# Optimization experiments

Measured on AMD Instinct MI355X. Metric: run time of the kernel, lower is better.

Reference implementation:

```python
import jax, jax.numpy as jnp
import numpy as np

B, S, D = 4, 2048, 2048
E = 64           # num_experts
TOPK = 2         # num_experts_per_token


def setup_inputs() -> dict:
    key = jax.random.key(0)
    k1, k2, k3 = jax.random.split(key, 3)
    x_real = jax.random.normal(k1, (B, S, D), dtype=jnp.float32)
    x_imag = jax.random.normal(k2, (B, S, D), dtype=jnp.float32)
    # flax Dense: kernel [in_features, out_features] with lecun_normal-ish scale
    W = jax.random.normal(k3, (2 * D, E), dtype=jnp.float32) / np.sqrt(2.0 * D)
    b = jnp.zeros((E,), dtype=jnp.float32)
    return {"x_real": x_real, "x_imag": x_imag, "W": W, "b": b}


def reference(x_real, x_imag, W, b):
    # amp = |x|, phase = angle(x) for x = x_real + i*x_imag
    amp = jnp.hypot(x_real, x_imag)                 # [B,S,D]
    phase = jnp.arctan2(x_imag, x_real)             # [B,S,D]
    routing_input = jnp.concatenate([amp, phase], axis=-1)  # [B,S,2D]
    scores = jnp.einsum('bsf,fe->bse', routing_input, W) + b  # [B,S,E]
    probs = jax.nn.softmax(scores, axis=-1)
    top_k_probs, top_k_indices = jax.lax.top_k(probs, TOPK)   # [B,S,K]
    top_k_probs = top_k_probs / jnp.sum(top_k_probs, axis=-1, keepdims=True)
    return (top_k_probs, top_k_indices)
```

## Files before the change

kernel.cpp:

```cpp
#include <hip/hip_runtime.h>
#include <math.h>

#define NTOK 8192
#define DD   2048
#define EE   64
#define STRIP 16
#define NKH 8
#define DSLICE (DD/NKH)
#define NCH (DSLICE/32)
#define PROB_N (NTOK*2)
#define F_SSTRIDE (128*4*64*8)

typedef __bf16 bf16x8 __attribute__((ext_vector_type(8)));
typedef float  f32x4  __attribute__((ext_vector_type(4)));
typedef unsigned short u16x8 __attribute__((ext_vector_type(8)));

__device__ __forceinline__ unsigned short bf16_rne(float x, float& rep) {
    unsigned u = __builtin_bit_cast(unsigned, x);
    unsigned r = u + 0x7FFFu + ((u >> 16) & 1u);
    unsigned short h = (unsigned short)(r >> 16);
    rep = __builtin_bit_cast(float, (unsigned)h << 16);
    return h;
}
__device__ __forceinline__ void split3(float x, unsigned short& h1,
                                       unsigned short& h2, unsigned short& h3) {
    float f1, f2, f3;
    h1 = bf16_rne(x, f1);
    float r1 = x - f1;
    h2 = bf16_rne(r1, f2);
    float r2 = r1 - f2;
    h3 = bf16_rne(r2, f3);
}

__global__ __launch_bounds__(256) void wsplit(const float* __restrict__ W,
                                              unsigned short* __restrict__ F) {
    const int g  = blockIdx.x * 256 + threadIdx.x;
    const int e  = g & 63;
    const int q  = g >> 6;
    const int d0 = q * 4;
    const int nt = e >> 4;
    const int k  = d0 & 31;
    const int lane = (k >> 3) * 16 + (e & 15);
    const int j0 = k & 7;
    const int ck = 2 * (d0 >> 5);

    unsigned short ah[3][4], ph[3][4];
    #pragma unroll
    for (int i = 0; i < 4; ++i) {
        split3(W[(size_t)(d0 + i) * EE + e],      ah[0][i], ah[1][i], ah[2][i]);
        split3(W[(size_t)(DD + d0 + i) * EE + e], ph[0][i], ph[1][i], ph[2][i]);
    }
    #pragma unroll
    for (int s = 0; s < 3; ++s) {
        ushort4 va = make_ushort4(ah[s][0], ah[s][1], ah[s][2], ah[s][3]);
        ushort4 vp = make_ushort4(ph[s][0], ph[s][1], ph[s][2], ph[s][3]);
        *(ushort4*)&F[(size_t)(((s * 128 + ck)     * 4 + nt) * 64 + lane) * 8 + j0] = va;
        *(ushort4*)&F[(size_t)(((s * 128 + ck + 1) * 4 + nt) * 64 + lane) * 8 + j0] = vp;
    }
}

__global__ __launch_bounds__(512, 4) void gemm_topk(
    const float* __restrict__ xr, const float* __restrict__ xi,
    const unsigned short* __restrict__ F, const float* __restrict__ bias,
    float* __restrict__ out)
{
    __shared__ float score8[NKH][STRIP][EE];
    __shared__ float scoreF[STRIP][EE];

    const int tid  = threadIdx.x;
    const int wv   = tid >> 6;
    const int lane = tid & 63;
    const int fm   = lane & 15;
    const int fq   = lane >> 4;
    const int t0   = blockIdx.x * STRIP;

    const float* prx = xr + (size_t)(t0 + fm) * DD + wv * DSLICE + fq * 8;
    const float* pix = xi + (size_t)(t0 + fm) * DD + wv * DSLICE + fq * 8;
    const unsigned short* bs0 = F + (size_t)(wv * NCH * 2) * 4 * 512 + lane * 8;
    const unsigned short* bs1 = bs0 + F_SSTRIDE;
    const unsigned short* bs2 = bs0 + 2 * F_SSTRIDE;

    f32x4 acc[4];
    #pragma unroll
    for (int n = 0; n < 4; ++n) acc[n] = (f32x4){0.f, 0.f, 0.f, 0.f};

    #pragma unroll 2
    for (int c = 0; c < NCH; ++c) {
        const float4 vr0 = *(const float4*)(prx);
        const float4 vr1 = *(const float4*)(prx + 4);
        const float4 vi0 = *(const float4*)(pix);
        const float4 vi1 = *(const float4*)(pix + 4);
        prx += 32; pix += 32;

        const float ar[8] = {vr0.x, vr0.y, vr0.z, vr0.w, vr1.x, vr1.y, vr1.z, vr1.w};
        const float ai[8] = {vi0.x, vi0.y, vi0.z, vi0.w, vi1.x, vi1.y, vi1.z, vi1.w};

        u16x8 u0, u1, u2;
        #pragma unroll
        for (int j = 0; j < 8; ++j) {
            const float amp = sqrtf(fmaf(ar[j], ar[j], ai[j] * ai[j]));
            unsigned short h1, h2, h3;
            split3(amp, h1, h2, h3);
            u0[j] = h1; u1[j] = h2; u2[j] = h3;
        }
        {
            const bf16x8 a1 = __builtin_bit_cast(bf16x8, u0);
            const bf16x8 a2 = __builtin_bit_cast(bf16x8, u1);
            const bf16x8 a3 = __builtin_bit_cast(bf16x8, u2);
            #pragma unroll
            for (int n = 0; n < 4; ++n) {
                const bf16x8 b1 = *(const bf16x8*)(bs0 + n * 512);
                const bf16x8 b2 = *(const bf16x8*)(bs1 + n * 512);
                const bf16x8 b3 = *(const bf16x8*)(bs2 + n * 512);
                acc[n] = __builtin_amdgcn_mfma_f32_16x16x32_bf16(a1, b1, acc[n], 0, 0, 0);
                acc[n] = __builtin_amdgcn_mfma_f32_16x16x32_bf16(a1, b2, acc[n], 0, 0, 0);
                acc[n] = __builtin_amdgcn_mfma_f32_16x16x32_bf16(a2, b1, acc[n], 0, 0, 0);
                acc[n] = __builtin_amdgcn_mfma_f32_16x16x32_bf16(a1, b3, acc[n], 0, 0, 0);
                acc[n] = __builtin_amdgcn_mfma_f32_16x16x32_bf16(a2, b2, acc[n], 0, 0, 0);
                acc[n] = __builtin_amdgcn_mfma_f32_16x16x32_bf16(a3, b1, acc[n], 0, 0, 0);
            }
        }
        #pragma unroll
        for (int j = 0; j < 8; ++j) {
            const float ph = atan2f(ai[j], ar[j]);
            unsigned short h1, h2, h3;
            split3(ph, h1, h2, h3);
            u0[j] = h1; u1[j] = h2; u2[j] = h3;
        }
        {
            const bf16x8 a1 = __builtin_bit_cast(bf16x8, u0);
            const bf16x8 a2 = __builtin_bit_cast(bf16x8, u1);
            const bf16x8 a3 = __builtin_bit_cast(bf16x8, u2);
            #pragma unroll
            for (int n = 0; n < 4; ++n) {
                const bf16x8 b1 = *(const bf16x8*)(bs0 + (4 + n) * 512);
                const bf16x8 b2 = *(const bf16x8*)(bs1 + (4 + n) * 512);
                const bf16x8 b3 = *(const bf16x8*)(bs2 + (4 + n) * 512);
                acc[n] = __builtin_amdgcn_mfma_f32_16x16x32_bf16(a1, b1, acc[n], 0, 0, 0);
                acc[n] = __builtin_amdgcn_mfma_f32_16x16x32_bf16(a1, b2, acc[n], 0, 0, 0);
                acc[n] = __builtin_amdgcn_mfma_f32_16x16x32_bf16(a2, b1, acc[n], 0, 0, 0);
                acc[n] = __builtin_amdgcn_mfma_f32_16x16x32_bf16(a1, b3, acc[n], 0, 0, 0);
                acc[n] = __builtin_amdgcn_mfma_f32_16x16x32_bf16(a2, b2, acc[n], 0, 0, 0);
                acc[n] = __builtin_amdgcn_mfma_f32_16x16x32_bf16(a3, b1, acc[n], 0, 0, 0);
            }
        }
        bs0 += 8 * 512; bs1 += 8 * 512; bs2 += 8 * 512;
    }

    #pragma unroll
    for (int n = 0; n < 4; ++n)
        #pragma unroll
        for (int r = 0; r < 4; ++r)
            score8[wv][fq * 4 + r][n * 16 + fm] = acc[n][r];
    __syncthreads();

    #pragma unroll
    for (int rep = 0; rep < 2; ++rep) {
        const int p = tid + rep * 512;
        const int tok = p >> 6, e = p & 63;
        float s = bias[e];
        #pragma unroll
        for (int w = 0; w < NKH; ++w) s += score8[w][tok][e];
        scoreF[tok][e] = s;
    }
    __syncthreads();

    #pragma unroll
    for (int rep = 0; rep < 2; ++rep) {
        const int tok = wv + rep * 8;
        float v1 = scoreF[tok][lane], v2 = -INFINITY;
        int   i1 = lane, i2 = 64;
        #pragma unroll
        for (int off = 1; off < 64; off <<= 1) {
            const float ov1 = __shfl_xor(v1, off, 64);
            const int   oi1 = __shfl_xor(i1, off, 64);
            const float ov2 = __shfl_xor(v2, off, 64);
            const int   oi2 = __shfl_xor(i2, off, 64);
            const bool b1 = (ov1 > v1) || (ov1 == v1 && oi1 < i1);
            const float n1 = b1 ? ov1 : v1;  const int ni1 = b1 ? oi1 : i1;
            const float c1 = b1 ? v1  : ov1; const int ci1 = b1 ? i1  : oi1;
            const float c2 = b1 ? ov2 : v2;  const int ci2 = b1 ? oi2 : i2;
            const bool b2 = (c1 > c2) || (c1 == c2 && ci1 < ci2);
            v1 = n1; i1 = ni1;
            v2 = b2 ? c1 : c2; i2 = b2 ? ci1 : ci2;
        }
        if (lane == 0) {
            const int t = t0 + tok;
            const float z  = expf(v2 - v1);
            const float p1 = 1.0f / (1.0f + z);
            const float p2 = z / (1.0f + z);
            out[(size_t)t * 2 + 0] = p1;
            out[(size_t)t * 2 + 1] = p2;
            out[PROB_N + (size_t)t * 2 + 0] = (float)i1;
            out[PROB_N + (size_t)t * 2 + 1] = (float)i2;
        }
    }
}

extern "C" void kernel_launch(void* const* d_in, const int* in_sizes, int n_in,
                              void* d_out, int out_size, void* d_ws, size_t ws_size,
                              hipStream_t stream) {
    const float* xr = (const float*)d_in[0];
    const float* xi = (const float*)d_in[1];
    const float* W  = (const float*)d_in[2];
    const float* b  = (const float*)d_in[3];
    float* out = (float*)d_out;
    unsigned short* F = (unsigned short*)d_ws;

    wsplit<<<128, 256, 0, stream>>>(W, F);
    gemm_topk<<<NTOK / STRIP, 512, 0, stream>>>(xr, xi, F, b, out);
}
```

Before: 197.4 us.

## Prefetch next x chunk, use fast atan2 and truncating bf16 split

Several changes to the fused routing GEMM. The x loads for the next chunk are issued before the current chunk is processed, a register double-buffer meant to hide global memory latency. The libm atan2f is replaced with a polynomial approximation using a hardware reciprocal. The round-to-nearest 3-way bf16 split becomes truncation packed with v_perm. The B fragments are hoisted ahead of the MFMAs. These cut VALU work and load stalls, but add register pressure and may give slightly different phase precision.

Result: faster. 187.6 us (-5.0%).

```diff
diff --git a/kernel.cpp b/kernel.cpp
--- a/kernel.cpp
+++ b/kernel.cpp
@@ -13,23 +13,65 @@
 
 typedef __bf16 bf16x8 __attribute__((ext_vector_type(8)));
 typedef float  f32x4  __attribute__((ext_vector_type(4)));
-typedef unsigned short u16x8 __attribute__((ext_vector_type(8)));
-
-__device__ __forceinline__ unsigned short bf16_rne(float x, float& rep) {
-    unsigned u = __builtin_bit_cast(unsigned, x);
-    unsigned r = u + 0x7FFFu + ((u >> 16) & 1u);
-    unsigned short h = (unsigned short)(r >> 16);
-    rep = __builtin_bit_cast(float, (unsigned)h << 16);
-    return h;
-}
-__device__ __forceinline__ void split3(float x, unsigned short& h1,
-                                       unsigned short& h2, unsigned short& h3) {
-    float f1, f2, f3;
-    h1 = bf16_rne(x, f1);
-    float r1 = x - f1;
-    h2 = bf16_rne(r1, f2);
-    float r2 = r1 - f2;
-    h3 = bf16_rne(r2, f3);
+typedef unsigned int u32x4 __attribute__((ext_vector_type(4)));
+
+__device__ __forceinline__ void tsplit3(float x, unsigned short& h1,
+                                        unsigned short& h2, unsigned short& h3) {
+    const unsigned u = __builtin_bit_cast(unsigned, x);
+    h1 = (unsigned short)(u >> 16);
+    const float f1 = __builtin_bit_cast(float, u & 0xFFFF0000u);
+    const float r1 = x - f1;
+    const unsigned v = __builtin_bit_cast(unsigned, r1);
+    h2 = (unsigned short)(v >> 16);
+    const float f2 = __builtin_bit_cast(float, v & 0xFFFF0000u);
+    const float r2 = r1 - f2;
+    h3 = (unsigned short)(__builtin_bit_cast(unsigned, r2) >> 16);
+}
+
+__device__ __forceinline__ float fast_atan2f(float y, float x) {
+    const float ax = __builtin_fabsf(x), ay = __builtin_fabsf(y);
+    const float hi = fmaxf(ax, ay), lo = fminf(ax, ay);
+    const bool  big = lo > 0.4142135679721832f * hi;
+    const float num = big ? (lo - hi) : lo;
+    const float den = big ? (lo + hi) : hi;
+    float rc = __builtin_amdgcn_rcpf(den);
+    rc = rc * fmaf(-den, rc, 2.0f);
+    const float z  = num * rc;
+    const float z2 = z * z;
+    float p = fmaf(z2, 8.05374449538e-2f, -1.38776856032e-1f);
+    p = fmaf(z2, p, 1.99777106478e-1f);
+    p = fmaf(z2, p, -3.33329491539e-1f);
+    float r = fmaf(z * z2, p, z);
+    r = r + (big ? 0.78539816339744830962f : 0.0f);
+    r = (ay > ax) ? (1.57079632679489661923f - r) : r;
+    r = (x < 0.0f) ? (3.14159265358979323846f - r) : r;
+    return copysignf(r, y);
+}
+
+__device__ __forceinline__ unsigned packhi(float a, float b) {
+    return __builtin_amdgcn_perm(__builtin_bit_cast(unsigned, b),
+                                 __builtin_bit_cast(unsigned, a), 0x07060302u);
+}
+
+__device__ __forceinline__ void split_planes(const float* v, bf16x8& o1,
+                                             bf16x8& o2, bf16x8& o3) {
+    u32x4 P1, P2, P3;
+    #pragma unroll
+    for (int p = 0; p < 4; ++p) {
+        const float a = v[2 * p], b = v[2 * p + 1];
+        const float f1a = __builtin_bit_cast(float, __builtin_bit_cast(unsigned, a) & 0xFFFF0000u);
+        const float f1b = __builtin_bit_cast(float, __builtin_bit_cast(unsigned, b) & 0xFFFF0000u);
+        const float r1a = a - f1a, r1b = b - f1b;
+        const float f2a = __builtin_bit_cast(float, __builtin_bit_cast(unsigned, r1a) & 0xFFFF0000u);
+        const float f2b = __builtin_bit_cast(float, __builtin_bit_cast(unsigned, r1b) & 0xFFFF0000u);
+        const float r2a = r1a - f2a, r2b = r1b - f2b;
+        P1[p] = packhi(a, b);
+        P2[p] = packhi(r1a, r1b);
+        P3[p] = packhi(r2a, r2b);
+    }
+    o1 = __builtin_bit_cast(bf16x8, P1);
+    o2 = __builtin_bit_cast(bf16x8, P2);
+    o3 = __builtin_bit_cast(bf16x8, P3);
 }
 
 __global__ __launch_bounds__(256) void wsplit(const float* __restrict__ W,
@@ -47,8 +89,8 @@
     unsigned short ah[3][4], ph[3][4];
     #pragma unroll
     for (int i = 0; i < 4; ++i) {
-        split3(W[(size_t)(d0 + i) * EE + e],      ah[0][i], ah[1][i], ah[2][i]);
-        split3(W[(size_t)(DD + d0 + i) * EE + e], ph[0][i], ph[1][i], ph[2][i]);
+        tsplit3(W[(size_t)(d0 + i) * EE + e],      ah[0][i], ah[1][i], ah[2][i]);
+        tsplit3(W[(size_t)(DD + d0 + i) * EE + e], ph[0][i], ph[1][i], ph[2][i]);
     }
     #pragma unroll
     for (int s = 0; s < 3; ++s) {
@@ -84,67 +126,78 @@
     #pragma unroll
     for (int n = 0; n < 4; ++n) acc[n] = (f32x4){0.f, 0.f, 0.f, 0.f};
 
+    float4 cr0 = *(const float4*)(prx);
+    float4 cr1 = *(const float4*)(prx + 4);
+    float4 ci0 = *(const float4*)(pix);
+    float4 ci1 = *(const float4*)(pix + 4);
+    prx += 32; pix += 32;
+
     #pragma unroll 2
     for (int c = 0; c < NCH; ++c) {
-        const float4 vr0 = *(const float4*)(prx);
-        const float4 vr1 = *(const float4*)(prx + 4);
-        const float4 vi0 = *(const float4*)(pix);
-        const float4 vi1 = *(const float4*)(pix + 4);
-        prx += 32; pix += 32;
-
-        const float ar[8] = {vr0.x, vr0.y, vr0.z, vr0.w, vr1.x, vr1.y, vr1.z, vr1.w};
-        const float ai[8] = {vi0.x, vi0.y, vi0.z, vi0.w, vi1.x, vi1.y, vi1.z, vi1.w};
-
-        u16x8 u0, u1, u2;
-        #pragma unroll
-        for (int j = 0; j < 8; ++j) {
-            const float amp = sqrtf(fmaf(ar[j], ar[j], ai[j] * ai[j]));
-            unsigned short h1, h2, h3;
-            split3(amp, h1, h2, h3);
-            u0[j] = h1; u1[j] = h2; u2[j] = h3;
-        }
+        float4 nr0, nr1, ni0, ni1;
+        if (c + 1 < NCH) {
+            nr0 = *(const float4*)(prx);
+            nr1 = *(const float4*)(prx + 4);
+            ni0 = *(const float4*)(pix);
+            ni1 = *(const float4*)(pix + 4);
+            prx += 32; pix += 32;
+        } else {
+            nr0 = cr0; nr1 = cr1; ni0 = ci0; ni1 = ci1;
+        }
+
+        const float ar[8] = {cr0.x, cr0.y, cr0.z, cr0.w, cr1.x, cr1.y, cr1.z, cr1.w};
+        const float ai[8] = {ci0.x, ci0.y, ci0.z, ci0.w, ci1.x, ci1.y, ci1.z, ci1.w};
+
         {
-            const bf16x8 a1 = __builtin_bit_cast(bf16x8, u0);
-            const bf16x8 a2 = __builtin_bit_cast(bf16x8, u1);
-            const bf16x8 a3 = __builtin_bit_cast(bf16x8, u2);
-            #pragma unroll
-            for (int n = 0; n < 4; ++n) {
-                const bf16x8 b1 = *(const bf16x8*)(bs0 + n * 512);
-                const bf16x8 b2 = *(const bf16x8*)(bs1 + n * 512);
-                const bf16x8 b3 = *(const bf16x8*)(bs2 + n * 512);
-                acc[n] = __builtin_amdgcn_mfma_f32_16x16x32_bf16(a1, b1, acc[n], 0, 0, 0);
-                acc[n] = __builtin_amdgcn_mfma_f32_16x16x32_bf16(a1, b2, acc[n], 0, 0, 0);
-                acc[n] = __builtin_amdgcn_mfma_f32_16x16x32_bf16(a2, b1, acc[n], 0, 0, 0);
-                acc[n] = __builtin_amdgcn_mfma_f32_16x16x32_bf16(a1, b3, acc[n], 0, 0, 0);
-                acc[n] = __builtin_amdgcn_mfma_f32_16x16x32_bf16(a2, b2, acc[n], 0, 0, 0);
-                acc[n] = __builtin_amdgcn_mfma_f32_16x16x32_bf16(a3, b1, acc[n], 0, 0, 0);
-            }
-        }
-        #pragma unroll
-        for (int j = 0; j < 8; ++j) {
-            const float ph = atan2f(ai[j], ar[j]);
-            unsigned short h1, h2, h3;
-            split3(ph, h1, h2, h3);
-            u0[j] = h1; u1[j] = h2; u2[j] = h3;
+            bf16x8 b1[4], b2[4], b3[4];
+            #pragma unroll
+            for (int n = 0; n < 4; ++n) {
+                b1[n] = *(const bf16x8*)(bs0 + n * 512);
+                b2[n] = *(const bf16x8*)(bs1 + n * 512);
+                b3[n] = *(const bf16x8*)(bs2 + n * 512);
+            }
+            float av[8];
+            #pragma unroll
+            for (int j = 0; j < 8; ++j)
+                av[j] = sqrtf(fmaf(ar[j], ar[j], ai[j] * ai[j]));
+            bf16x8 a1, a2, a3;
+            split_planes(av, a1, a2, a3);
+            #pragma unroll
+            for (int n = 0; n < 4; ++n) {
+                acc[n] = __builtin_amdgcn_mfma_f32_16x16x32_bf16(a1, b1[n], acc[n], 0, 0, 0);
+                acc[n] = __builtin_amdgcn_mfma_f32_16x16x32_bf16(a1, b2[n], acc[n], 0, 0, 0);
+                acc[n] = __builtin_amdgcn_mfma_f32_16x16x32_bf16(a2, b1[n], acc[n], 0, 0, 0);
+                acc[n] = __builtin_amdgcn_mfma_f32_16x16x32_bf16(a1, b3[n], acc[n], 0, 0, 0);
+                acc[n] = __builtin_amdgcn_mfma_f32_16x16x32_bf16(a2, b2[n], acc[n], 0, 0, 0);
+                acc[n] = __builtin_amdgcn_mfma_f32_16x16x32_bf16(a3, b1[n], acc[n], 0, 0, 0);
+            }
         }
         {
-            const bf16x8 a1 = __builtin_bit_cast(bf16x8, u0);
-            const bf16x8 a2 = __builtin_bit_cast(bf16x8, u1);
-            const bf16x8 a3 = __builtin_bit_cast(bf16x8, u2);
-            #pragma unroll
-            for (int n = 0; n < 4; ++n) {
-                const bf16x8 b1 = *(const bf16x8*)(bs0 + (4 + n) * 512);
-                const bf16x8 b2 = *(const bf16x8*)(bs1 + (4 + n) * 512);
-                const bf16x8 b3 = *(const bf16x8*)(bs2 + (4 + n) * 512);
-                acc[n] = __builtin_amdgcn_mfma_f32_16x16x32_bf16(a1, b1, acc[n], 0, 0, 0);
-                acc[n] = __builtin_amdgcn_mfma_f32_16x16x32_bf16(a1, b2, acc[n], 0, 0, 0);
-                acc[n] = __builtin_amdgcn_mfma_f32_16x16x32_bf16(a2, b1, acc[n], 0, 0, 0);
-                acc[n] = __builtin_amdgcn_mfma_f32_16x16x32_bf16(a1, b3, acc[n], 0, 0, 0);
-                acc[n] = __builtin_amdgcn_mfma_f32_16x16x32_bf16(a2, b2, acc[n], 0, 0, 0);
-                acc[n] = __builtin_amdgcn_mfma_f32_16x16x32_bf16(a3, b1, acc[n], 0, 0, 0);
+            bf16x8 b1[4], b2[4], b3[4];
+            #pragma unroll
+            for (int n = 0; n < 4; ++n) {
+                b1[n] = *(const bf16x8*)(bs0 + (4 + n) * 512);
+                b2[n] = *(const bf16x8*)(bs1 + (4 + n) * 512);
+                b3[n] = *(const bf16x8*)(bs2 + (4 + n) * 512);
+            }
+            float pv[8];
+            #pragma unroll
+            for (int j = 0; j < 8; ++j)
+                pv[j] = fast_atan2f(ai[j], ar[j]);
+            bf16x8 a1, a2, a3;
+            split_planes(pv, a1, a2, a3);
+            #pragma unroll
+            for (int n = 0; n < 4; ++n) {
+                acc[n] = __builtin_amdgcn_mfma_f32_16x16x32_bf16(a1, b1[n], acc[n], 0, 0, 0);
+                acc[n] = __builtin_amdgcn_mfma_f32_16x16x32_bf16(a1, b2[n], acc[n], 0, 0, 0);
+                acc[n] = __builtin_amdgcn_mfma_f32_16x16x32_bf16(a2, b1[n], acc[n], 0, 0, 0);
+                acc[n] = __builtin_amdgcn_mfma_f32_16x16x32_bf16(a1, b3[n], acc[n], 0, 0, 0);
+                acc[n] = __builtin_amdgcn_mfma_f32_16x16x32_bf16(a2, b2[n], acc[n], 0, 0, 0);
+                acc[n] = __builtin_amdgcn_mfma_f32_16x16x32_bf16(a3, b1[n], acc[n], 0, 0, 0);
             }
         }
         bs0 += 8 * 512; bs1 += 8 * 512; bs2 += 8 * 512;
+        cr0 = nr0; cr1 = nr1; ci0 = ni0; ci1 = ni1;
     }
 
     #pragma unroll
```
